# Kernel optimization log

Hardware: AMD Instinct MI355X
Metric: run time of the kernel (lower is better)

The kernel has to match this reference:

```python
import jax, jax.numpy as jnp
import numpy as np

SENSOR_H, SENSOR_W = 256, 256
SPP = 16
BATCH, C, H_IMG, W_IMG = 4, 3, 1024, 1024


def setup_inputs() -> dict:
    key = jax.random.key(0)
    k1, k2 = jax.random.split(key)
    img = jax.random.uniform(k1, (BATCH, C, H_IMG, W_IMG), dtype=jnp.float32)
    jitter = jax.random.uniform(k2, (SPP, SENSOR_H, SENSOR_W, 2), dtype=jnp.float32)
    t = jnp.ones((1,), jnp.float32)
    return {"img": img, "t": t, "jitter": jitter}


def deform(pos, t):
    # Analytic per-axis foveation diffeomorphism [-1,1]^2 -> [-1,1]^2:
    #   f(u) = tanh(t*u)/tanh(t), f'(u) = t*(1 - tanh(t*u)^2)/tanh(t)
    # Jacobian is diagonal, so det = f'(x) * f'(y).
    tt = t[0]
    s = jnp.tanh(tt)
    th = jnp.tanh(tt * pos)
    warped = th / s                      # (..., 2)
    dd = tt * (1.0 - th * th) / s        # diagonal Jacobian entries (..., 2)
    det = dd[..., 0] * dd[..., 1]        # (...)
    return warped, det


def grid_sample_border(img, grid):
    # img: (b,c,H,W); grid: (spp,h,w,2) in [-1,1]
    # bilinear, padding_mode='border', align_corners=False (matches F.grid_sample)
    b, c, H, W = img.shape
    gx = (grid[..., 0] + 1.0) * (W / 2.0) - 0.5
    gy = (grid[..., 1] + 1.0) * (H / 2.0) - 0.5
    gx = jnp.clip(gx, 0.0, W - 1.0)
    gy = jnp.clip(gy, 0.0, H - 1.0)
    x0 = jnp.floor(gx)
    y0 = jnp.floor(gy)
    wx = (gx - x0)[None, None]           # (1,1,spp,h,w)
    wy = (gy - y0)[None, None]
    x0i = jnp.clip(x0.astype(jnp.int32), 0, W - 1)
    y0i = jnp.clip(y0.astype(jnp.int32), 0, H - 1)
    x1i = jnp.clip(x0i + 1, 0, W - 1)
    y1i = jnp.clip(y0i + 1, 0, H - 1)
    # fancy-index gather: result (b,c,spp,h,w); avoids tiling img over (b*spp)
    v00 = img[:, :, y0i, x0i]
    v01 = img[:, :, y0i, x1i]
    v10 = img[:, :, y1i, x0i]
    v11 = img[:, :, y1i, x1i]
    return (v00 * (1 - wx) * (1 - wy) + v01 * wx * (1 - wy)
            + v10 * (1 - wx) * wy + v11 * wx * wy)


def reference(img, t, jitter):
    step_x = 2.0 / SENSOR_W
    step_y = 2.0 / SENSOR_H
    px = jnp.arange(-1.0, 1.0, step_x, dtype=jnp.float32)
    py = jnp.arange(-1.0, 1.0, step_y, dtype=jnp.float32)
    gx, gy = jnp.meshgrid(px, py, indexing='xy')          # (h, w)
    pixel_pos = jnp.stack((gx, gy), axis=-1)[None]        # (1, h, w, 2)
    jit = jitter * jnp.array([step_x, step_y], jnp.float32)
    pos = pixel_pos + jit                                 # (spp, h, w, 2)
    warped, det = deform(pos, t)                          # (spp,h,w,2), (spp,h,w)
    samples = grid_sample_border(img, warped)             # (b, c, spp, h, w)
    weighted = jnp.mean(samples * det[None, None], axis=2)  # (b, c, h, w)
    area = jnp.mean(det, axis=0)[None, None]              # (1, 1, h, w)
    return weighted / area
```

## Files before the change

### kernel.cpp

```cpp
#include <hip/hip_runtime.h>
#include <hip/hip_fp16.h>

#define SPP   16
#define SH    256
#define SW    256
#define HI    1024
#define WI    1024
#define CH    3
#define BATCH 4

#define TS    16
#define MAXD  88

__device__ __forceinline__ float fast_tanh(float x) {
    const float e = __expf(2.0f * x);
    return (e - 1.0f) * __builtin_amdgcn_rcpf(e + 1.0f);
}

__global__ __launch_bounds__(256) void foveated_tile(
    const float* __restrict__ img,
    const float* __restrict__ t_ptr,
    const float* __restrict__ jitter,
    float* __restrict__ out)
{
    __shared__ uint2 lds[MAXD * MAXD];

    const int bid  = blockIdx.x;
    const int L    = (bid & 7) * 128 + (bid >> 3);
    const int b    = L >> 8;
    const int trow = (L >> 4) & 15;
    const int tcol = L & 15;
    const int sx0  = tcol * TS;
    const int sy0  = trow * TS;

    const float step  = 2.0f / 256.0f;
    const float tt    = t_ptr[0];
    const float inv_s = __builtin_amdgcn_rcpf(fast_tanh(tt));

    auto gmap = [&](float p) {
        float g = (fast_tanh(tt * p) * inv_s + 1.0f) * 512.0f - 0.5f;
        return fminf(fmaxf(g, 0.0f), 1023.0f);
    };
    const float pxmin = -1.0f + sx0 * step, pxmax = pxmin + TS * step;
    const float pymin = -1.0f + sy0 * step, pymax = pymin + TS * step;
    const int x_lo = max((int)gmap(pxmin) - 1, 0);
    const int x_hi = min((int)gmap(pxmax) + 2, WI - 1);
    const int y_lo = max((int)gmap(pymin) - 1, 0);
    const int y_hi = min((int)gmap(pymax) + 2, HI - 1);
    const int ncols = x_hi - x_lo + 1;
    const int nrows = y_hi - y_lo + 1;
    const bool fits = (ncols <= MAXD) && (nrows <= MAXD);

    const size_t plane = (size_t)HI * WI;
    const float* __restrict__ p0 = img + (size_t)(b * CH) * plane;
    const float* __restrict__ p1 = p0 + plane;
    const float* __restrict__ p2 = p1 + plane;

    const int th = threadIdx.x;
    const int sx = sx0 + (th & 15);
    const int sy = sy0 + (th >> 4);

    const float px = -1.0f + sx * step;
    const float py = -1.0f + sy * step;

    float acc0 = 0.0f, acc1 = 0.0f, acc2 = 0.0f, dsum = 0.0f;

    const float2* __restrict__ jit2 = (const float2*)jitter;
    const int jbase = sy * SW + sx;

    if (fits) {
        const int npix = nrows * ncols;
        const unsigned mdiv = (1u << 22) / (unsigned)ncols + 1u;
        for (int i = th; i < npix; i += 256) {
            const int r = (int)(((unsigned)i * mdiv) >> 22);
            const int c = i - r * ncols;
            const int g = (y_lo + r) * WI + (x_lo + c);
            union { __half2 h[2]; uint2 u; } v;
            v.h[0] = __floats2half2_rn(p0[g], p1[g]);
            v.h[1] = __floats2half2_rn(p2[g], 0.0f);
            lds[r * MAXD + c] = v.u;
        }
        __syncthreads();

        #pragma unroll 4
        for (int sp = 0; sp < SPP; ++sp) {
            const float2 j = jit2[sp * (SH * SW) + jbase];
            const float posx = px + j.x * step;
            const float posy = py + j.y * step;

            const float thx = fast_tanh(tt * posx);
            const float thy = fast_tanh(tt * posy);
            const float ddx = tt * (1.0f - thx * thx) * inv_s;
            const float ddy = tt * (1.0f - thy * thy) * inv_s;
            const float det = ddx * ddy;

            float gx = (thx * inv_s + 1.0f) * 512.0f - 0.5f;
            float gy = (thy * inv_s + 1.0f) * 512.0f - 0.5f;
            gx = fminf(fmaxf(gx, 0.0f), (float)(WI - 1));
            gy = fminf(fmaxf(gy, 0.0f), (float)(HI - 1));

            const int xb = min((int)gx, WI - 2);
            const int yb = min((int)gy, HI - 2);
            const float fx = gx - (float)xb;
            const float fy = gy - (float)yb;

            const float w00 = (1.0f - fx) * (1.0f - fy) * det;
            const float w01 = fx * (1.0f - fy) * det;
            const float w10 = (1.0f - fx) * fy * det;
            const float w11 = fx * fy * det;
            dsum += det;

            const int lidx = (yb - y_lo) * MAXD + (xb - x_lo);
            const uint2 q00 = lds[lidx];
            const uint2 q01 = lds[lidx + 1];
            const uint2 q10 = lds[lidx + MAXD];
            const uint2 q11 = lds[lidx + MAXD + 1];

            const float2 a00 = __half22float2(*(const __half2*)&q00.x);
            const float2 b00 = __half22float2(*(const __half2*)&q00.y);
            const float2 a01 = __half22float2(*(const __half2*)&q01.x);
            const float2 b01 = __half22float2(*(const __half2*)&q01.y);
            const float2 a10 = __half22float2(*(const __half2*)&q10.x);
            const float2 b10 = __half22float2(*(const __half2*)&q10.y);
            const float2 a11 = __half22float2(*(const __half2*)&q11.x);
            const float2 b11 = __half22float2(*(const __half2*)&q11.y);

            acc0 += w00 * a00.x + w01 * a01.x + w10 * a10.x + w11 * a11.x;
            acc1 += w00 * a00.y + w01 * a01.y + w10 * a10.y + w11 * a11.y;
            acc2 += w00 * b00.x + w01 * b01.x + w10 * b10.x + w11 * b11.x;
        }
    } else {
        #pragma unroll 4
        for (int sp = 0; sp < SPP; ++sp) {
            const float2 j = jit2[sp * (SH * SW) + jbase];
            const float posx = px + j.x * step;
            const float posy = py + j.y * step;

            const float thx = fast_tanh(tt * posx);
            const float thy = fast_tanh(tt * posy);
            const float ddx = tt * (1.0f - thx * thx) * inv_s;
            const float ddy = tt * (1.0f - thy * thy) * inv_s;
            const float det = ddx * ddy;

            float gx = (thx * inv_s + 1.0f) * 512.0f - 0.5f;
            float gy = (thy * inv_s + 1.0f) * 512.0f - 0.5f;
            gx = fminf(fmaxf(gx, 0.0f), (float)(WI - 1));
            gy = fminf(fmaxf(gy, 0.0f), (float)(HI - 1));

            const int xb = min((int)gx, WI - 2);
            const int yb = min((int)gy, HI - 2);
            const float fx = gx - (float)xb;
            const float fy = gy - (float)yb;

            const float w00 = (1.0f - fx) * (1.0f - fy) * det;
            const float w01 = fx * (1.0f - fy) * det;
            const float w10 = (1.0f - fx) * fy * det;
            const float w11 = fx * fy * det;
            dsum += det;

            const int i0 = yb * WI + xb;
            const int i1 = i0 + WI;
            { const float2 a = *(const float2*)(p0 + i0), c = *(const float2*)(p0 + i1);
              acc0 += a.x * w00 + a.y * w01 + c.x * w10 + c.y * w11; }
            { const float2 a = *(const float2*)(p1 + i0), c = *(const float2*)(p1 + i1);
              acc1 += a.x * w00 + a.y * w01 + c.x * w10 + c.y * w11; }
            { const float2 a = *(const float2*)(p2 + i0), c = *(const float2*)(p2 + i1);
              acc2 += a.x * w00 + a.y * w01 + c.x * w10 + c.y * w11; }
        }
    }

    const float inv_d = 1.0f / dsum;
    const int pix = sy * SW + sx;
    const size_t ob = (size_t)b * CH * (SH * SW) + pix;
    out[ob]                 = acc0 * inv_d;
    out[ob + (SH * SW)]     = acc1 * inv_d;
    out[ob + 2 * (SH * SW)] = acc2 * inv_d;
}

extern "C" void kernel_launch(void* const* d_in, const int* in_sizes, int n_in,
                              void* d_out, int out_size, void* d_ws, size_t ws_size,
                              hipStream_t stream) {
    const float* img    = (const float*)d_in[0];
    const float* t      = (const float*)d_in[1];
    const float* jitter = (const float*)d_in[2];
    float* out          = (float*)d_out;

    hipLaunchKernelGGL(foveated_tile, dim3(1024), dim3(256), 0, stream,
                       img, t, jitter, out);
}
```

Baseline: 116.5 us.

## Split samples across thread pairs and shrink LDS tile to 6 bytes per texel

Each output pixel is now handled by two threads, each doing 8 of the 16 samples, with partial sums combined by a lane shuffle. Blocks grow to 512 threads so the cooperative LDS tile fill has twice the loaders. The LDS layout changes from 8 bytes per texel (padded uint2) to a half2 array plus a separate half array, cutting LDS use so more blocks fit per CU. In exchange, the interleaved jitter access pattern changes coalescing, each texel now needs two separate LDS reads, and the final store needs an extra shuffle reduction.

```diff
diff --git a/kernel.cpp b/kernel.cpp
--- a/kernel.cpp
+++ b/kernel.cpp
@@ -11,19 +11,21 @@
 
 #define TS    16
 #define MAXD  88
+#define NTHR  512
 
 __device__ __forceinline__ float fast_tanh(float x) {
     const float e = __expf(2.0f * x);
     return (e - 1.0f) * __builtin_amdgcn_rcpf(e + 1.0f);
 }
 
-__global__ __launch_bounds__(256) void foveated_tile(
+__global__ __launch_bounds__(NTHR, 6) void foveated_tile(
     const float* __restrict__ img,
     const float* __restrict__ t_ptr,
     const float* __restrict__ jitter,
     float* __restrict__ out)
 {
-    __shared__ uint2 lds[MAXD * MAXD];
+    __shared__ __half2 lds_rg[MAXD * MAXD];
+    __shared__ __half  lds_b [MAXD * MAXD];
 
     const int bid  = blockIdx.x;
     const int L    = (bid & 7) * 128 + (bid >> 3);
@@ -57,8 +59,10 @@
     const float* __restrict__ p2 = p1 + plane;
 
     const int th = threadIdx.x;
-    const int sx = sx0 + (th & 15);
-    const int sy = sy0 + (th >> 4);
+    const int h  = th & 1;
+    const int p  = th >> 1;
+    const int sx = sx0 + (p & 15);
+    const int sy = sy0 + (p >> 4);
 
     const float px = -1.0f + sx * step;
     const float py = -1.0f + sy * step;
@@ -66,25 +70,23 @@
     float acc0 = 0.0f, acc1 = 0.0f, acc2 = 0.0f, dsum = 0.0f;
 
     const float2* __restrict__ jit2 = (const float2*)jitter;
-    const int jbase = sy * SW + sx;
+    const int jbase = h * 8 * (SH * SW) + sy * SW + sx;
 
     if (fits) {
         const int npix = nrows * ncols;
         const unsigned mdiv = (1u << 22) / (unsigned)ncols + 1u;
-        for (int i = th; i < npix; i += 256) {
+        for (int i = th; i < npix; i += NTHR) {
             const int r = (int)(((unsigned)i * mdiv) >> 22);
             const int c = i - r * ncols;
             const int g = (y_lo + r) * WI + (x_lo + c);
-            union { __half2 h[2]; uint2 u; } v;
-            v.h[0] = __floats2half2_rn(p0[g], p1[g]);
-            v.h[1] = __floats2half2_rn(p2[g], 0.0f);
-            lds[r * MAXD + c] = v.u;
+            lds_rg[r * MAXD + c] = __floats2half2_rn(p0[g], p1[g]);
+            lds_b [r * MAXD + c] = __float2half_rn(p2[g]);
         }
         __syncthreads();
 
-        #pragma unroll 4
-        for (int sp = 0; sp < SPP; ++sp) {
-            const float2 j = jit2[sp * (SH * SW) + jbase];
+        #pragma unroll 2
+        for (int k = 0; k < 8; ++k) {
+            const float2 j = jit2[k * (SH * SW) + jbase];
             const float posx = px + j.x * step;
             const float posy = py + j.y * step;
 
@@ -111,28 +113,23 @@
             dsum += det;
 
             const int lidx = (yb - y_lo) * MAXD + (xb - x_lo);
-            const uint2 q00 = lds[lidx];
-            const uint2 q01 = lds[lidx + 1];
-            const uint2 q10 = lds[lidx + MAXD];
-            const uint2 q11 = lds[lidx + MAXD + 1];
+            const float2 f00 = __half22float2(lds_rg[lidx]);
+            const float2 f01 = __half22float2(lds_rg[lidx + 1]);
+            const float2 f10 = __half22float2(lds_rg[lidx + MAXD]);
+            const float2 f11 = __half22float2(lds_rg[lidx + MAXD + 1]);
+            const float v00 = __half2float(lds_b[lidx]);
+            const float v01 = __half2float(lds_b[lidx + 1]);
+            const float v10 = __half2float(lds_b[lidx + MAXD]);
+            const float v11 = __half2float(lds_b[lidx + MAXD + 1]);
 
-            const float2 a00 = __half22float2(*(const __half2*)&q00.x);
-            const float2 b00 = __half22float2(*(const __half2*)&q00.y);
-            const float2 a01 = __half22float2(*(const __half2*)&q01.x);
-            const float2 b01 = __half22float2(*(const __half2*)&q01.y);
-            const float2 a10 = __half22float2(*(const __half2*)&q10.x);
-            const float2 b10 = __half22float2(*(const __half2*)&q10.y);
-            const float2 a11 = __half22float2(*(const __half2*)&q11.x);
-            const float2 b11 = __half22float2(*(const __half2*)&q11.y);
-
-            acc0 += w00 * a00.x + w01 * a01.x + w10 * a10.x + w11 * a11.x;
-            acc1 += w00 * a00.y + w01 * a01.y + w10 * a10.y + w11 * a11.y;
-            acc2 += w00 * b00.x + w01 * b01.x + w10 * b10.x + w11 * b11.x;
+            acc0 += w00 * f00.x + w01 * f01.x + w10 * f10.x + w11 * f11.x;
+            acc1 += w00 * f00.y + w01 * f01.y + w10 * f10.y + w11 * f11.y;
+            acc2 += w00 * v00   + w01 * v01   + w10 * v10   + w11 * v11;
         }
     } else {
-        #pragma unroll 4
-        for (int sp = 0; sp < SPP; ++sp) {
-            const float2 j = jit2[sp * (SH * SW) + jbase];
+        #pragma unroll 2
+        for (int k = 0; k < 8; ++k) {
+            const float2 j = jit2[k * (SH * SW) + jbase];
             const float posx = px + j.x * step;
             const float posy = py + j.y * step;
 
@@ -160,21 +157,28 @@
 
             const int i0 = yb * WI + xb;
             const int i1 = i0 + WI;
-            { const float2 a = *(const float2*)(p0 + i0), c = *(const float2*)(p0 + i1);
-              acc0 += a.x * w00 + a.y * w01 + c.x * w10 + c.y * w11; }
-            { const float2 a = *(const float2*)(p1 + i0), c = *(const float2*)(p1 + i1);
-              acc1 += a.x * w00 + a.y * w01 + c.x * w10 + c.y * w11; }
-            { const float2 a = *(const float2*)(p2 + i0), c = *(const float2*)(p2 + i1);
-              acc2 += a.x * w00 + a.y * w01 + c.x * w10 + c.y * w11; }
+            { const float2 a = *(const float2*)(p0 + i0), c2 = *(const float2*)(p0 + i1);
+              acc0 += a.x * w00 + a.y * w01 + c2.x * w10 + c2.y * w11; }
+            { const float2 a = *(const float2*)(p1 + i0), c2 = *(const float2*)(p1 + i1);
+              acc1 += a.x * w00 + a.y * w01 + c2.x * w10 + c2.y * w11; }
+            { const float2 a = *(const float2*)(p2 + i0), c2 = *(const float2*)(p2 + i1);
+              acc2 += a.x * w00 + a.y * w01 + c2.x * w10 + c2.y * w11; }
         }
     }
 
-    const float inv_d = 1.0f / dsum;
-    const int pix = sy * SW + sx;
-    const size_t ob = (size_t)b * CH * (SH * SW) + pix;
-    out[ob]                 = acc0 * inv_d;
-    out[ob + (SH * SW)]     = acc1 * inv_d;
-    out[ob + 2 * (SH * SW)] = acc2 * inv_d;
+    acc0 += __shfl_xor(acc0, 1);
+    acc1 += __shfl_xor(acc1, 1);
+    acc2 += __shfl_xor(acc2, 1);
+    dsum += __shfl_xor(dsum, 1);
+
+    if (h == 0) {
+        const float inv_d = 1.0f / dsum;
+        const int pix = sy * SW + sx;
+        const size_t ob = (size_t)b * CH * (SH * SW) + pix;
+        out[ob]                 = acc0 * inv_d;
+        out[ob + (SH * SW)]     = acc1 * inv_d;
+        out[ob + 2 * (SH * SW)] = acc2 * inv_d;
+    }
 }
 
 extern "C" void kernel_launch(void* const* d_in, const int* in_sizes, int n_in,
@@ -185,6 +189,6 @@
     const float* jitter = (const float*)d_in[2];
     float* out          = (float*)d_out;
 
-    hipLaunchKernelGGL(foveated_tile, dim3(1024), dim3(256), 0, stream,
+    hipLaunchKernelGGL(foveated_tile, dim3(1024), dim3(NTHR), 0, stream,
                        img, t, jitter, out);
 }
```

Measured after the change: 108.1 us. -7.2%, faster.

## Give each wavefront a 4x4 tile and split samples across lanes

Applied to the files above, without the earlier changes.

Work is redistributed so each 64-lane wavefront owns a 4x4 sensor tile with its own private LDS patch. Four lanes share each output pixel and each handles 4 of the 16 samples, and the partial sums are combined with xor-shuffles. The block-wide barrier becomes a wave-local lgkmcnt wait, the jitter loads are hoisted, and the grid grows to 8192 blocks of 128 threads to raise occupancy and parallelism. The cost is more redundant halo loads per output, since small tiles reload overlapping image regions, plus the shuffle-reduction overhead.

```diff
diff --git a/kernel.cpp b/kernel.cpp
--- a/kernel.cpp
+++ b/kernel.cpp
@@ -9,27 +9,35 @@
 #define CH    3
 #define BATCH 4
 
-#define TS    16
-#define MAXD  88
+#define TS    4
+#define MAXD  26
+#define LSTR  27
+#define NTHR  128
 
 __device__ __forceinline__ float fast_tanh(float x) {
     const float e = __expf(2.0f * x);
     return (e - 1.0f) * __builtin_amdgcn_rcpf(e + 1.0f);
 }
 
-__global__ __launch_bounds__(256) void foveated_tile(
+__global__ __launch_bounds__(NTHR, 7) void foveated_wave4(
     const float* __restrict__ img,
     const float* __restrict__ t_ptr,
     const float* __restrict__ jitter,
     float* __restrict__ out)
 {
-    __shared__ uint2 lds[MAXD * MAXD];
+    __shared__ uint2 lds_px[2][MAXD * LSTR];
 
     const int bid  = blockIdx.x;
-    const int L    = (bid & 7) * 128 + (bid >> 3);
-    const int b    = L >> 8;
-    const int trow = (L >> 4) & 15;
-    const int tcol = L & 15;
+    const int Lb   = (bid & 7) * 1024 + (bid >> 3);
+    const int th   = threadIdx.x;
+    const int w    = th >> 6;
+    const int lane = th & 63;
+
+    const int tile = Lb * 2 + w;
+    const int b    = tile >> 12;
+    const int rem  = tile & 4095;
+    const int trow = rem >> 6;
+    const int tcol = rem & 63;
     const int sx0  = tcol * TS;
     const int sy0  = trow * TS;
 
@@ -49,132 +57,154 @@
     const int y_hi = min((int)gmap(pymax) + 2, HI - 1);
     const int ncols = x_hi - x_lo + 1;
     const int nrows = y_hi - y_lo + 1;
-    const bool fits = (ncols <= MAXD) && (nrows <= MAXD);
+    const bool fits = (ncols > 0) && (nrows > 0) &&
+                      (ncols <= MAXD) && (nrows <= MAXD);
 
     const size_t plane = (size_t)HI * WI;
     const float* __restrict__ p0 = img + (size_t)(b * CH) * plane;
     const float* __restrict__ p1 = p0 + plane;
     const float* __restrict__ p2 = p1 + plane;
 
-    const int th = threadIdx.x;
-    const int sx = sx0 + (th & 15);
-    const int sy = sy0 + (th >> 4);
+    const int p  = lane >> 2;
+    const int q  = lane & 3;
+    const int sx = sx0 + (p & 3);
+    const int sy = sy0 + (p >> 2);
 
     const float px = -1.0f + sx * step;
     const float py = -1.0f + sy * step;
 
+    const float2* __restrict__ jit2 = (const float2*)jitter;
+    const int jbase = (q * 4) * (SH * SW) + sy * SW + sx;
+    const float2 jv0 = jit2[jbase];
+    const float2 jv1 = jit2[jbase + 1 * (SH * SW)];
+    const float2 jv2 = jit2[jbase + 2 * (SH * SW)];
+    const float2 jv3 = jit2[jbase + 3 * (SH * SW)];
+
     float acc0 = 0.0f, acc1 = 0.0f, acc2 = 0.0f, dsum = 0.0f;
 
-    const float2* __restrict__ jit2 = (const float2*)jitter;
-    const int jbase = sy * SW + sx;
+    uint2* __restrict__ T = lds_px[w];
+
+    auto sample_lds = [&](float jx, float jy) {
+        const float posx = px + jx * step;
+        const float posy = py + jy * step;
+
+        const float thx = fast_tanh(tt * posx);
+        const float thy = fast_tanh(tt * posy);
+        const float ddx = tt * (1.0f - thx * thx) * inv_s;
+        const float ddy = tt * (1.0f - thy * thy) * inv_s;
+        const float det = ddx * ddy;
+
+        float gx = (thx * inv_s + 1.0f) * 512.0f - 0.5f;
+        float gy = (thy * inv_s + 1.0f) * 512.0f - 0.5f;
+        gx = fminf(fmaxf(gx, 0.0f), (float)(WI - 1));
+        gy = fminf(fmaxf(gy, 0.0f), (float)(HI - 1));
+
+        const int xb = min((int)gx, WI - 2);
+        const int yb = min((int)gy, HI - 2);
+        const float fx = gx - (float)xb;
+        const float fy = gy - (float)yb;
+
+        const float w00 = (1.0f - fx) * (1.0f - fy) * det;
+        const float w01 = fx * (1.0f - fy) * det;
+        const float w10 = (1.0f - fx) * fy * det;
+        const float w11 = fx * fy * det;
+        dsum += det;
+
+        const int lidx = (yb - y_lo) * LSTR + (xb - x_lo);
+        const uint2 q00 = T[lidx];
+        const uint2 q01 = T[lidx + 1];
+        const uint2 q10 = T[lidx + LSTR];
+        const uint2 q11 = T[lidx + LSTR + 1];
+
+        const float2 a00 = __half22float2(*(const __half2*)&q00.x);
+        const float2 b00 = __half22float2(*(const __half2*)&q00.y);
+        const float2 a01 = __half22float2(*(const __half2*)&q01.x);
+        const float2 b01 = __half22float2(*(const __half2*)&q01.y);
+        const float2 a10 = __half22float2(*(const __half2*)&q10.x);
+        const float2 b10 = __half22float2(*(const __half2*)&q10.y);
+        const float2 a11 = __half22float2(*(const __half2*)&q11.x);
+        const float2 b11 = __half22float2(*(const __half2*)&q11.y);
+
+        acc0 += w00 * a00.x + w01 * a01.x + w10 * a10.x + w11 * a11.x;
+        acc1 += w00 * a00.y + w01 * a01.y + w10 * a10.y + w11 * a11.y;
+        acc2 += w00 * b00.x + w01 * b01.x + w10 * b10.x + w11 * b11.x;
+    };
+
+    auto sample_glb = [&](float jx, float jy) {
+        const float posx = px + jx * step;
+        const float posy = py + jy * step;
+
+        const float thx = fast_tanh(tt * posx);
+        const float thy = fast_tanh(tt * posy);
+        const float ddx = tt * (1.0f - thx * thx) * inv_s;
+        const float ddy = tt * (1.0f - thy * thy) * inv_s;
+        const float det = ddx * ddy;
+
+        float gx = (thx * inv_s + 1.0f) * 512.0f - 0.5f;
+        float gy = (thy * inv_s + 1.0f) * 512.0f - 0.5f;
+        gx = fminf(fmaxf(gx, 0.0f), (float)(WI - 1));
+        gy = fminf(fmaxf(gy, 0.0f), (float)(HI - 1));
+
+        const int xb = min((int)gx, WI - 2);
+        const int yb = min((int)gy, HI - 2);
+        const float fx = gx - (float)xb;
+        const float fy = gy - (float)yb;
+
+        const float w00 = (1.0f - fx) * (1.0f - fy) * det;
+        const float w01 = fx * (1.0f - fy) * det;
+        const float w10 = (1.0f - fx) * fy * det;
+        const float w11 = fx * fy * det;
+        dsum += det;
+
+        const int i0 = yb * WI + xb;
+        const int i1 = i0 + WI;
+        { const float a0 = p0[i0], a1 = p0[i0 + 1], c0 = p0[i1], c1 = p0[i1 + 1];
+          acc0 += a0 * w00 + a1 * w01 + c0 * w10 + c1 * w11; }
+        { const float a0 = p1[i0], a1 = p1[i0 + 1], c0 = p1[i1], c1 = p1[i1 + 1];
+          acc1 += a0 * w00 + a1 * w01 + c0 * w10 + c1 * w11; }
+        { const float a0 = p2[i0], a1 = p2[i0 + 1], c0 = p2[i1], c1 = p2[i1 + 1];
+          acc2 += a0 * w00 + a1 * w01 + c0 * w10 + c1 * w11; }
+    };
 
     if (fits) {
         const int npix = nrows * ncols;
         const unsigned mdiv = (1u << 22) / (unsigned)ncols + 1u;
-        for (int i = th; i < npix; i += 256) {
+        for (int i = lane; i < npix; i += 64) {
             const int r = (int)(((unsigned)i * mdiv) >> 22);
             const int c = i - r * ncols;
             const int g = (y_lo + r) * WI + (x_lo + c);
             union { __half2 h[2]; uint2 u; } v;
             v.h[0] = __floats2half2_rn(p0[g], p1[g]);
             v.h[1] = __floats2half2_rn(p2[g], 0.0f);
-            lds[r * MAXD + c] = v.u;
+            T[r * LSTR + c] = v.u;
         }
-        __syncthreads();
-
-        #pragma unroll 4
-        for (int sp = 0; sp < SPP; ++sp) {
-            const float2 j = jit2[sp * (SH * SW) + jbase];
-            const float posx = px + j.x * step;
-            const float posy = py + j.y * step;
-
-            const float thx = fast_tanh(tt * posx);
-            const float thy = fast_tanh(tt * posy);
-            const float ddx = tt * (1.0f - thx * thx) * inv_s;
-            const float ddy = tt * (1.0f - thy * thy) * inv_s;
-            const float det = ddx * ddy;
-
-            float gx = (thx * inv_s + 1.0f) * 512.0f - 0.5f;
-            float gy = (thy * inv_s + 1.0f) * 512.0f - 0.5f;
-            gx = fminf(fmaxf(gx, 0.0f), (float)(WI - 1));
-            gy = fminf(fmaxf(gy, 0.0f), (float)(HI - 1));
-
-            const int xb = min((int)gx, WI - 2);
-            const int yb = min((int)gy, HI - 2);
-            const float fx = gx - (float)xb;
-            const float fy = gy - (float)yb;
-
-            const float w00 = (1.0f - fx) * (1.0f - fy) * det;
-            const float w01 = fx * (1.0f - fy) * det;
-            const float w10 = (1.0f - fx) * fy * det;
-            const float w11 = fx * fy * det;
-            dsum += det;
-
-            const int lidx = (yb - y_lo) * MAXD + (xb - x_lo);
-            const uint2 q00 = lds[lidx];
-            const uint2 q01 = lds[lidx + 1];
-            const uint2 q10 = lds[lidx + MAXD];
-            const uint2 q11 = lds[lidx + MAXD + 1];
-
-            const float2 a00 = __half22float2(*(const __half2*)&q00.x);
-            const float2 b00 = __half22float2(*(const __half2*)&q00.y);
-            const float2 a01 = __half22float2(*(const __half2*)&q01.x);
-            const float2 b01 = __half22float2(*(const __half2*)&q01.y);
-            const float2 a10 = __half22float2(*(const __half2*)&q10.x);
-            const float2 b10 = __half22float2(*(const __half2*)&q10.y);
-            const float2 a11 = __half22float2(*(const __half2*)&q11.x);
-            const float2 b11 = __half22float2(*(const __half2*)&q11.y);
-
-            acc0 += w00 * a00.x + w01 * a01.x + w10 * a10.x + w11 * a11.x;
-            acc1 += w00 * a00.y + w01 * a01.y + w10 * a10.y + w11 * a11.y;
-            acc2 += w00 * b00.x + w01 * b01.x + w10 * b10.x + w11 * b11.x;
-        }
+        asm volatile("s_waitcnt lgkmcnt(0)" ::: "memory");
+        __builtin_amdgcn_sched_barrier(0);
+
+        sample_lds(jv0.x, jv0.y);
+        sample_lds(jv1.x, jv1.y);
+        sample_lds(jv2.x, jv2.y);
+        sample_lds(jv3.x, jv3.y);
     } else {
-        #pragma unroll 4
-        for (int sp = 0; sp < SPP; ++sp) {
-            const float2 j = jit2[sp * (SH * SW) + jbase];
-            const float posx = px + j.x * step;
-            const float posy = py + j.y * step;
-
-            const float thx = fast_tanh(tt * posx);
-            const float thy = fast_tanh(tt * posy);
-            const float ddx = tt * (1.0f - thx * thx) * inv_s;
-            const float ddy = tt * (1.0f - thy * thy) * inv_s;
-            const float det = ddx * ddy;
-
-            float gx = (thx * inv_s + 1.0f) * 512.0f - 0.5f;
-            float gy = (thy * inv_s + 1.0f) * 512.0f - 0.5f;
-            gx = fminf(fmaxf(gx, 0.0f), (float)(WI - 1));
-            gy = fminf(fmaxf(gy, 0.0f), (float)(HI - 1));
-
-            const int xb = min((int)gx, WI - 2);
-            const int yb = min((int)gy, HI - 2);
-            const float fx = gx - (float)xb;
-            const float fy = gy - (float)yb;
-
-            const float w00 = (1.0f - fx) * (1.0f - fy) * det;
-            const float w01 = fx * (1.0f - fy) * det;
-            const float w10 = (1.0f - fx) * fy * det;
-            const float w11 = fx * fy * det;
-            dsum += det;
-
-            const int i0 = yb * WI + xb;
-            const int i1 = i0 + WI;
-            { const float2 a = *(const float2*)(p0 + i0), c = *(const float2*)(p0 + i1);
-              acc0 += a.x * w00 + a.y * w01 + c.x * w10 + c.y * w11; }
-            { const float2 a = *(const float2*)(p1 + i0), c = *(const float2*)(p1 + i1);
-              acc1 += a.x * w00 + a.y * w01 + c.x * w10 + c.y * w11; }
-            { const float2 a = *(const float2*)(p2 + i0), c = *(const float2*)(p2 + i1);
-              acc2 += a.x * w00 + a.y * w01 + c.x * w10 + c.y * w11; }
-        }
+        sample_glb(jv0.x, jv0.y);
+        sample_glb(jv1.x, jv1.y);
+        sample_glb(jv2.x, jv2.y);
+        sample_glb(jv3.x, jv3.y);
     }
 
-    const float inv_d = 1.0f / dsum;
-    const int pix = sy * SW + sx;
-    const size_t ob = (size_t)b * CH * (SH * SW) + pix;
-    out[ob]                 = acc0 * inv_d;
-    out[ob + (SH * SW)]     = acc1 * inv_d;
-    out[ob + 2 * (SH * SW)] = acc2 * inv_d;
+    acc0 += __shfl_xor(acc0, 1);  acc0 += __shfl_xor(acc0, 2);
+    acc1 += __shfl_xor(acc1, 1);  acc1 += __shfl_xor(acc1, 2);
+    acc2 += __shfl_xor(acc2, 1);  acc2 += __shfl_xor(acc2, 2);
+    dsum += __shfl_xor(dsum, 1);  dsum += __shfl_xor(dsum, 2);
+
+    if (q == 0) {
+        const float inv_d = 1.0f / dsum;
+        const int pix = sy * SW + sx;
+        const size_t ob = (size_t)b * CH * (SH * SW) + pix;
+        out[ob]                 = acc0 * inv_d;
+        out[ob + (SH * SW)]     = acc1 * inv_d;
+        out[ob + 2 * (SH * SW)] = acc2 * inv_d;
+    }
 }
 
 extern "C" void kernel_launch(void* const* d_in, const int* in_sizes, int n_in,
@@ -185,6 +215,6 @@
     const float* jitter = (const float*)d_in[2];
     float* out          = (float*)d_out;
 
-    hipLaunchKernelGGL(foveated_tile, dim3(1024), dim3(256), 0, stream,
+    hipLaunchKernelGGL(foveated_wave4, dim3(8192), dim3(NTHR), 0, stream,
                        img, t, jitter, out);
 }
```

After: 108.1 us. -7.2%, faster.
